# Kernel tuning notes

Measured on AMD Instinct MI355X. Metric: run time of the kernel, lower is better.

## Reference

```python
import jax, jax.numpy as jnp
import numpy as np

B, T, HID = 2, 2048, 2048
NH, NKV, HD = 32, 8, 64


def setup_inputs() -> dict:
    key = jax.random.key(0)
    ks = jax.random.split(key, 5)
    x = jax.random.normal(ks[0], (B, T, HID), dtype=jnp.float32)
    position_ids = jnp.broadcast_to(jnp.arange(T, dtype=jnp.int32), (B, T))
    s = 0.02
    Wq = jax.random.normal(ks[1], (NH * HD, HID), dtype=jnp.float32) * s
    Wk = jax.random.normal(ks[2], (NKV * HD, HID), dtype=jnp.float32) * s
    Wv = jax.random.normal(ks[3], (NKV * HD, HID), dtype=jnp.float32) * s
    Wo = jax.random.normal(ks[4], (HID, NH * HD), dtype=jnp.float32) * s
    return {"x": x, "position_ids": position_ids, "Wq": Wq, "Wk": Wk, "Wv": Wv, "Wo": Wo}


def _rotate_half(t):
    t1, t2 = jnp.split(t, 2, axis=-1)
    return jnp.concatenate([-t2, t1], axis=-1)


def reference(x, position_ids, Wq, Wk, Wv, Wo):
    Bd, Td, _ = x.shape
    q = (x @ Wq.T).reshape(Bd, Td, NH, HD)
    k = (x @ Wk.T).reshape(Bd, Td, NKV, HD)
    v = (x @ Wv.T).reshape(Bd, Td, NKV, HD)

    # DummyRotaryEmbedding: freqs over even indices, repeat_interleave(2)
    freqs = 1.0 / (10000.0 ** (jnp.arange(0, HD, 2, dtype=jnp.float32) / HD))
    angles = position_ids.astype(jnp.float32)[:, :, None] * freqs  # [B,T,HD/2]
    cos = jnp.repeat(jnp.cos(angles), 2, axis=-1)[:, :, None, :]   # [B,T,1,HD]
    sin = jnp.repeat(jnp.sin(angles), 2, axis=-1)[:, :, None, :]

    q = q * cos + _rotate_half(q) * sin
    k = k * cos + _rotate_half(k) * sin

    n_rep = NH // NKV
    k = jnp.repeat(k, n_rep, axis=2)  # [B,T,NH,HD]
    v = jnp.repeat(v, n_rep, axis=2)

    scale = 1.0 / np.sqrt(HD).astype(np.float32)
    scores = jnp.einsum('bqhd,bkhd->bhqk', q, k) * scale  # [B,NH,T,T]
    probs = jax.nn.softmax(scores, axis=-1)
    out = jnp.einsum('bhqk,bkhd->bqhd', probs, v).reshape(Bd, Td, NH * HD)
    return out @ Wo.T
```

## Files before the change

kernel.cpp:

```cpp
#include <hip/hip_runtime.h>
#include <hip/hip_bf16.h>
#include <stdint.h>


typedef __attribute__((ext_vector_type(8))) short short8;
typedef __attribute__((ext_vector_type(4))) float f32x4;
typedef __attribute__((ext_vector_type(16))) float f32x16;

__device__ __forceinline__ unsigned short f2bf(float f) {
  union { float f; uint32_t u; } x; x.f = f;
  uint32_t r = x.u + 0x7fffu + ((x.u >> 16) & 1u);
  return (unsigned short)(r >> 16);
}
__device__ __forceinline__ float bf2f(unsigned short u) {
  union { uint32_t u; float f; } x; x.u = ((uint32_t)u) << 16;
  return x.f;
}
__device__ __forceinline__ uint32_t cvt_pk_bf16(float a, float b) {
  uint32_t r;
  asm("v_cvt_pk_bf16_f32 %0, %1, %2" : "=v"(r) : "v"(a), "v"(b));
  return r;
}
__device__ __forceinline__ void pl32swap(uint32_t& dst, uint32_t& src) {
  asm("v_permlane32_swap_b32 %0, %1" : "+v"(dst), "+v"(src));
}

__device__ __forceinline__ void gload_lds16(const void* g, void* l) {
  __builtin_amdgcn_global_load_lds(
      (const __attribute__((address_space(1))) unsigned int*)g,
      (__attribute__((address_space(3))) unsigned int*)l, 16, 0, 0);
}

#define VMCNT(n) asm volatile("s_waitcnt vmcnt(" #n ")" ::: "memory")
#define LGKMCNT0 asm volatile("s_waitcnt lgkmcnt(0)" ::: "memory")

__global__ __launch_bounds__(256) void convert_kernel(
    const float* __restrict__ x, const float* __restrict__ Wq,
    const float* __restrict__ Wk, const float* __restrict__ Wv,
    const float* __restrict__ Wo,
    unsigned short* __restrict__ xb, unsigned short* __restrict__ wqkvb,
    unsigned short* __restrict__ wob) {
  const int NX = 1048576;
  const int NQ = 524288;
  const int NK = 131072;
  const int NV = 131072;
  const int NO = 524288;
  const int total = NX + NQ + NK + NV + NO;
  for (int i = blockIdx.x * blockDim.x + threadIdx.x; i < total;
       i += gridDim.x * blockDim.x) {
    const float4* s; unsigned short* d; int o;
    if (i < NX)                 { o = i;               s = (const float4*)x;  d = xb; }
    else if (i < NX+NQ)         { o = i-NX;            s = (const float4*)Wq; d = wqkvb; }
    else if (i < NX+NQ+NK)      { o = i-NX-NQ;         s = (const float4*)Wk; d = wqkvb + 4194304; }
    else if (i < NX+NQ+NK+NV)   { o = i-NX-NQ-NK;      s = (const float4*)Wv; d = wqkvb + 5242880; }
    else                        { o = i-NX-NQ-NK-NV;   s = (const float4*)Wo; d = wob; }
    float4 v0 = s[(size_t)o * 2];
    float4 v1 = s[(size_t)o * 2 + 1];
    short8 r;
    r[0] = (short)f2bf(v0.x); r[1] = (short)f2bf(v0.y);
    r[2] = (short)f2bf(v0.z); r[3] = (short)f2bf(v0.w);
    r[4] = (short)f2bf(v1.x); r[5] = (short)f2bf(v1.y);
    r[6] = (short)f2bf(v1.z); r[7] = (short)f2bf(v1.w);
    *(short8*)(d + (size_t)o * 8) = r;
  }
}

template <int NQ, typename OutT>
__global__ __launch_bounds__(512, 2) void gemm_2cu(
    const unsigned short* __restrict__ A, const unsigned short* __restrict__ Bt,
    OutT* __restrict__ C, int N, int K) {
  __shared__ unsigned short lA[2][128 * 64];
  __shared__ unsigned short lB[2][NQ * 64 * 64];
  const int tid  = threadIdx.x;
  const int lane = tid & 63;
  const int w    = tid >> 6;
  const int wr   = w >> 2, wc = w & 3;
  const long tm  = (long)blockIdx.y * 128;
  const long tn  = (long)blockIdx.x * (NQ * 64);

  f32x4 acc[4][NQ];
#pragma unroll
  for (int fi = 0; fi < 4; ++fi)
#pragma unroll
    for (int nq = 0; nq < NQ; ++nq) acc[fi][nq] = (f32x4){0.f, 0.f, 0.f, 0.f};

  const int srow = tid >> 3;
  const int sgr  = ((tid & 7) ^ (srow & 7)) * 8;
  const unsigned short* ga = A  + (tm + srow) * (long)K + sgr;
  const unsigned short* gb = Bt + (tn + srow) * (long)K + sgr;

  int aoff[4][2], boff[NQ][2];
#pragma unroll
  for (int fi = 0; fi < 4; ++fi)
#pragma unroll
    for (int ks = 0; ks < 2; ++ks) {
      int gk = (lane >> 4) + ks * 4;
      aoff[fi][ks] = (wr * 64 + fi * 16 + (lane & 15)) * 128 + ((gk ^ (lane & 7)) << 4);
    }
#pragma unroll
  for (int nq = 0; nq < NQ; ++nq)
#pragma unroll
    for (int ks = 0; ks < 2; ++ks) {
      int gk = (lane >> 4) + ks * 4;
      boff[nq][ks] = (wc * (NQ * 16) + nq * 16 + (lane & 15)) * 128 + ((gk ^ (lane & 7)) << 4);
    }

#pragma unroll
  for (int i = 0; i < 2; ++i)  gload_lds16(ga + (long)(64 * i) * K, &lA[0][tid * 8 + 4096 * i]);
#pragma unroll
  for (int i = 0; i < NQ; ++i) gload_lds16(gb + (long)(64 * i) * K, &lB[0][tid * 8 + 4096 * i]);
  VMCNT(0);
  __builtin_amdgcn_s_barrier();

  const int nk = K >> 6;
  for (int t = 0; t < nk; ++t) {
    const int slot = t & 1;
    const unsigned short* gaT = ga + (long)((t + 1) << 6);
    const unsigned short* gbT = gb + (long)((t + 1) << 6);
    const bool st = (t + 1 < nk);
    const char* As = (const char*)lA[slot];
    const char* Bs = (const char*)lB[slot];
    unsigned short* dA = &lA[slot ^ 1][tid * 8];
    unsigned short* dB = &lB[slot ^ 1][tid * 8];

    short8 af[4][2];
#pragma unroll
    for (int nq = 0; nq < NQ; ++nq) {
      if (nq == 0) {
#pragma unroll
        for (int fi = 0; fi < 4; ++fi)
#pragma unroll
          for (int ks = 0; ks < 2; ++ks)
            af[fi][ks] = *(const short8*)(As + aoff[fi][ks]);
      }
      short8 bf0 = *(const short8*)(Bs + boff[nq][0]);
      short8 bf1 = *(const short8*)(Bs + boff[nq][1]);
      if (st && nq == 0) {
        gload_lds16(gaT,                 dA);
        gload_lds16(gaT + (long)64 * K,  dA + 4096);
#pragma unroll
        for (int i = 0; i < NQ; ++i)
          gload_lds16(gbT + (long)(64 * i) * K, dB + 4096 * i);
      }
      __builtin_amdgcn_s_barrier();
      LGKMCNT0;
      __builtin_amdgcn_sched_barrier(0);
      __builtin_amdgcn_s_setprio(1);
#pragma unroll
      for (int fi = 0; fi < 4; ++fi)
        acc[fi][nq] = __builtin_amdgcn_mfma_f32_16x16x32_bf16(af[fi][0], bf0, acc[fi][nq], 0, 0, 0);
#pragma unroll
      for (int fi = 0; fi < 4; ++fi)
        acc[fi][nq] = __builtin_amdgcn_mfma_f32_16x16x32_bf16(af[fi][1], bf1, acc[fi][nq], 0, 0, 0);
      __builtin_amdgcn_s_setprio(0);
      __builtin_amdgcn_sched_barrier(0);
      if (nq == NQ - 1) VMCNT(0);
      __builtin_amdgcn_s_barrier();
    }
  }

#pragma unroll
  for (int fi = 0; fi < 4; ++fi)
#pragma unroll
    for (int nq = 0; nq < NQ; ++nq) {
      long col = tn + wc * (NQ * 16) + nq * 16 + (lane & 15);
#pragma unroll
      for (int i = 0; i < 4; ++i) {
        long row = tm + wr * 64 + fi * 16 + (lane >> 4) * 4 + i;
        float v = acc[fi][nq][i];
        if constexpr (sizeof(OutT) == 2) C[row * N + col] = (OutT)f2bf(v);
        else                             C[row * N + col] = (OutT)v;
      }
    }
}

__global__ __launch_bounds__(256) void rope_kernel(
    unsigned short* __restrict__ qkv, const int* __restrict__ pos_ids) {
  const int m = blockIdx.x;
  const int tid = threadIdx.x;
  const float QSCALE = 0.18033688011112042f;
  __shared__ float cs[32], sn[32];
  if (tid < 32) {
    float pos = (float)pos_ids[m];
    float a = pos * exp2f(-(float)tid * 0.4152410118609203f);
    float s_, c_;
    sincosf(a, &s_, &c_);
    cs[tid] = c_; sn[tid] = s_;
  }
  __syncthreads();
  unsigned short* row = qkv + (size_t)m * 3072;

  const int qc = tid * 8;
  short8 qa = *(const short8*)(row + qc);
  short8 qp = *(const short8*)(row + (qc ^ 32));
  short8 ka = {}, kp = {};
  if (tid < 64) {
    const int kc = 2048 + tid * 8;
    ka = *(const short8*)(row + kc);
    kp = *(const short8*)(row + (kc ^ 32));
  }
  __syncthreads();

  {
    const int dbase = qc & 63;
    const float sgn = (qc & 32) ? 1.0f : -1.0f;
    short8 out;
#pragma unroll
    for (int j = 0; j < 8; ++j) {
      int fi = (dbase + j) >> 1;
      float o = bf2f((unsigned short)qa[j]) * cs[fi] +
                sgn * bf2f((unsigned short)qp[j]) * sn[fi];
      out[j] = (short)f2bf(o * QSCALE);
    }
    *(short8*)(row + qc) = out;
  }
  if (tid < 64) {
    const int kc = 2048 + tid * 8;
    const int dbase = (tid * 8) & 63;
    const float sgn = ((tid * 8) & 32) ? 1.0f : -1.0f;
    short8 out;
#pragma unroll
    for (int j = 0; j < 8; ++j) {
      int fi = (dbase + j) >> 1;
      float o = bf2f((unsigned short)ka[j]) * cs[fi] +
                sgn * bf2f((unsigned short)kp[j]) * sn[fi];
      out[j] = (short)f2bf(o);
    }
    *(short8*)(row + kc) = out;
  }
}

__global__ __launch_bounds__(256) void vtrans_kernel(
    const unsigned short* __restrict__ qkv, unsigned short* __restrict__ Vt) {
  const int tb = blockIdx.x, g = blockIdx.y, b = blockIdx.z;
  const int tid = threadIdx.x;
  __shared__ unsigned short lt[64 * 72];

  {
    const int r = tid >> 2, c = (tid & 3) * 16;
    const unsigned short* src =
        qkv + ((size_t)(b * 2048 + tb * 64 + r)) * 3072 + 2560 + g * 64 + c;
    short8 v0 = *(const short8*)(src);
    short8 v1 = *(const short8*)(src + 8);
    *(short8*)&lt[r * 72 + c] = v0;
    *(short8*)&lt[r * 72 + c + 8] = v1;
  }
  __syncthreads();

  {
    const int d = tid >> 2, t0 = (tid & 3) * 16;
    short8 o0, o1;
#pragma unroll
    for (int j = 0; j < 8; ++j) o0[j] = (short)lt[(t0 + j) * 72 + d];
#pragma unroll
    for (int j = 0; j < 8; ++j) o1[j] = (short)lt[(t0 + 8 + j) * 72 + d];
    unsigned short* dst =
        Vt + ((size_t)((b * 8 + g) * 64 + d)) * 2048 + tb * 64 + t0;
    *(short8*)(dst) = o0;
    *(short8*)(dst + 8) = o1;
  }
}

__global__ __launch_bounds__(512) void attn_kernel(
    const unsigned short* __restrict__ qkv,
    const unsigned short* __restrict__ Vt,
    unsigned short* __restrict__ attnout) {
  const int qt = blockIdx.x, g = blockIdx.y, b = blockIdx.z;
  const int tid = threadIdx.x, lane = tid & 63, w = tid >> 6;
  const int l31 = lane & 31, hi = lane >> 5;
  const int h = g * 4 + (w & 3);
  const int qbase = qt * 64 + (w >> 2) * 32;

  __shared__ unsigned short lK[3][64 * 64];
  __shared__ unsigned short lV[4][64 * 64];

  short8 qf[4];
  {
    const unsigned short* qrow =
        qkv + ((size_t)(b * 2048 + qbase + l31)) * 3072 + h * 64 + hi * 8;
#pragma unroll
    for (int kc = 0; kc < 4; ++kc) qf[kc] = *(const short8*)(qrow + kc * 16);
  }

  f32x16 o0, o1, zro;
#pragma unroll
  for (int i = 0; i < 16; ++i) { o0[i] = 0.f; o1[i] = 0.f; zro[i] = 0.f; }
  float lrun = 0.f;

  const unsigned short* kgbase = qkv + (size_t)b * 2048 * 3072 + 2048 + g * 64;
  const unsigned short* vgbase = Vt + ((size_t)(b * 8 + g) * 64) * 2048;
  const int srow = w * 8 + (lane >> 3);
  const int sg = ((lane & 7) ^ (srow & 7)) * 8;

  int koff[2][4];
#pragma unroll
  for (int s = 0; s < 2; ++s)
#pragma unroll
    for (int kc = 0; kc < 4; ++kc) {
      int r = s * 32 + l31;
      koff[s][kc] = r * 128 + (((kc * 2 + hi) ^ (r & 7)) << 4);
    }

#define STAGE(kbuf, vbuf, kb)                                                       \
  {                                                                                 \
    const unsigned short* kk_ = kgbase + (size_t)((kb) * 64) * 3072;                \
    const unsigned short* vv_ = vgbase + (kb) * 64;                                 \
    gload_lds16(kk_ + (size_t)srow * 3072 + sg, &lK[kbuf][(w * 8) * 64]);           \
    gload_lds16(vv_ + (size_t)srow * 2048 + sg, &lV[vbuf][(w * 8) * 64]);           \
  }

#define PV_BLOCK(VBASE)                                                             \
  {                                                                                 \
    const char* Vb_ = (VBASE);                                                      \
    _Pragma("unroll")                                                               \
    for (int ks = 0; ks < 2; ++ks) {                                                \
      union { uint32_t u[4]; short8 s8; } fa, fb;                                   \
      _Pragma("unroll")                                                             \
      for (int u = 0; u < 4; ++u) { fa.u[u] = wd[ks][u]; fb.u[u] = wd[ks][4 + u]; } \
      const int kk0 = ks * 2, kk1 = ks * 2 + 1;                                     \
      short8 va0 = *(const short8*)(Vb_ + koff[0][kk0]);                            \
      short8 va1 = *(const short8*)(Vb_ + koff[1][kk0]);                            \
      o0 = __builtin_amdgcn_mfma_f32_32x32x16_bf16(fa.s8, va0, o0, 0, 0, 0);        \
      o1 = __builtin_amdgcn_mfma_f32_32x32x16_bf16(fa.s8, va1, o1, 0, 0, 0);        \
      short8 vb0 = *(const short8*)(Vb_ + koff[0][kk1]);                            \
      short8 vb1 = *(const short8*)(Vb_ + koff[1][kk1]);                            \
      o0 = __builtin_amdgcn_mfma_f32_32x32x16_bf16(fb.s8, vb0, o0, 0, 0, 0);        \
      o1 = __builtin_amdgcn_mfma_f32_32x32x16_bf16(fb.s8, vb1, o1, 0, 0, 0);        \
    }                                                                               \
  }

  uint32_t wd[2][8];

  STAGE(0, 0, 0);
  STAGE(1, 1, 1);
  VMCNT(2);
  __builtin_amdgcn_s_barrier();
  __builtin_amdgcn_sched_barrier(0);

  int kcur = 0;
  int kst  = 2;
#pragma unroll 1
  for (int t = 0; t < 32; ++t) {
    if (t < 30) STAGE(kst, (t + 2) & 3, t + 2);
    const char* Kb = (const char*)lK[kcur];

    f32x16 s0, s1;
    __builtin_amdgcn_s_setprio(1);
    {
      short8 k0 = *(const short8*)(Kb + koff[0][0]);
      short8 k1 = *(const short8*)(Kb + koff[1][0]);
      s0 = __builtin_amdgcn_mfma_f32_32x32x16_bf16(k0, qf[0], zro, 0, 0, 0);
      s1 = __builtin_amdgcn_mfma_f32_32x32x16_bf16(k1, qf[0], zro, 0, 0, 0);
    }
#pragma unroll
    for (int kc = 1; kc < 4; ++kc) {
      short8 k0 = *(const short8*)(Kb + koff[0][kc]);
      short8 k1 = *(const short8*)(Kb + koff[1][kc]);
      s0 = __builtin_amdgcn_mfma_f32_32x32x16_bf16(k0, qf[kc], s0, 0, 0, 0);
      s1 = __builtin_amdgcn_mfma_f32_32x32x16_bf16(k1, qf[kc], s1, 0, 0, 0);
    }
    if (t > 0) PV_BLOCK((const char*)lV[(t - 1) & 3]);
    __builtin_amdgcn_s_setprio(0);

#pragma unroll
    for (int i = 0; i < 16; ++i) { s0[i] = __builtin_amdgcn_exp2f(s0[i]); lrun += s0[i]; }
#pragma unroll
    for (int i = 0; i < 16; ++i) { s1[i] = __builtin_amdgcn_exp2f(s1[i]); lrun += s1[i]; }

#pragma unroll
    for (int mi = 0; mi < 8; ++mi) {
      wd[0][mi] = cvt_pk_bf16(s0[2 * mi], s0[2 * mi + 1]);
      wd[1][mi] = cvt_pk_bf16(s1[2 * mi], s1[2 * mi + 1]);
    }
#pragma unroll
    for (int ks = 0; ks < 2; ++ks) {
      pl32swap(wd[ks][0], wd[ks][2]);
      pl32swap(wd[ks][1], wd[ks][3]);
      pl32swap(wd[ks][4], wd[ks][6]);
      pl32swap(wd[ks][5], wd[ks][7]);
    }

    if (t < 30) { VMCNT(2); } else { VMCNT(0); }
    __builtin_amdgcn_s_barrier();
    __builtin_amdgcn_sched_barrier(0);

    kcur = (kcur == 2) ? 0 : kcur + 1;
    kst  = (kst == 2) ? 0 : kst + 1;
  }

  PV_BLOCK((const char*)lV[3]);

  lrun += __shfl_xor(lrun, 32);
  float inv = 1.0f / lrun;
  const size_t obase =
      (size_t)(b * 2048 + qbase) * 2048 + h * 64 + l31;
#pragma unroll
  for (int reg = 0; reg < 16; ++reg) {
    int q = (reg & 3) + 8 * (reg >> 2) + 4 * hi;
    float invq = __shfl(inv, q);
    attnout[obase + (size_t)q * 2048]      = f2bf(o0[reg] * invq);
    attnout[obase + (size_t)q * 2048 + 32] = f2bf(o1[reg] * invq);
  }
#undef STAGE
#undef PV_BLOCK
}

extern "C" void kernel_launch(void* const* d_in, const int* in_sizes, int n_in,
                              void* d_out, int out_size, void* d_ws, size_t ws_size,
                              hipStream_t stream) {
  (void)in_sizes; (void)n_in; (void)out_size; (void)ws_size;
  const float* x  = (const float*)d_in[0];
  const int* pos  = (const int*)d_in[1];
  const float* Wq = (const float*)d_in[2];
  const float* Wk = (const float*)d_in[3];
  const float* Wv = (const float*)d_in[4];
  const float* Wo = (const float*)d_in[5];
  float* out = (float*)d_out;
  char* ws = (char*)d_ws;

  unsigned short* xb      = (unsigned short*)(ws);
  unsigned short* wqkvb   = (unsigned short*)(ws + 16777216);
  unsigned short* wob     = (unsigned short*)(ws + 29360128);
  unsigned short* qkv     = (unsigned short*)(ws + 37748736);
  unsigned short* Vt      = (unsigned short*)(ws + 62914560);
  unsigned short* attnout = (unsigned short*)(ws + 67108864);

  convert_kernel<<<2048, 256, 0, stream>>>(x, Wq, Wk, Wv, Wo, xb, wqkvb, wob);
  gemm_2cu<3, unsigned short><<<dim3(16, 32), 512, 0, stream>>>(xb, wqkvb, qkv, 3072, 2048);
  rope_kernel<<<4096, 256, 0, stream>>>(qkv, pos);
  vtrans_kernel<<<dim3(32, 8, 2), 256, 0, stream>>>(qkv, Vt);
  attn_kernel<<<dim3(32, 8, 2), 512, 0, stream>>>(qkv, Vt, attnout);
  gemm_2cu<2, float><<<dim3(16, 32), 512, 0, stream>>>(attnout, wob, out, 2048, 2048);
}
```

Measured before the change: 195.9 us.

## Fuse fp32-to-bf16 weight conversion into GEMM B-operand loading

The weight conversion pass in the convert kernel is removed. Both GEMMs now read fp32 weights directly into registers, convert them to bf16 with packed cvt, and write them to LDS, double-buffered against the MFMA loop. This drops a separate read and write of about 10 MB of weights and shrinks the convert launch. In exchange, each GEMM block reads twice as many B bytes and repeats the conversion, because the weights are re-read by every M-tile block (32 row tiles). The B path also moves from async global_load_lds to register loads plus VALU work that must finish before the barrier.

Result: slower. 224.8 us (+14.8%).

```diff
diff --git a/kernel.cpp b/kernel.cpp
--- a/kernel.cpp
+++ b/kernel.cpp
@@ -35,39 +35,26 @@
 #define LGKMCNT0 asm volatile("s_waitcnt lgkmcnt(0)" ::: "memory")
 
 __global__ __launch_bounds__(256) void convert_kernel(
-    const float* __restrict__ x, const float* __restrict__ Wq,
-    const float* __restrict__ Wk, const float* __restrict__ Wv,
-    const float* __restrict__ Wo,
-    unsigned short* __restrict__ xb, unsigned short* __restrict__ wqkvb,
-    unsigned short* __restrict__ wob) {
+    const float* __restrict__ x, unsigned short* __restrict__ xb) {
   const int NX = 1048576;
-  const int NQ = 524288;
-  const int NK = 131072;
-  const int NV = 131072;
-  const int NO = 524288;
-  const int total = NX + NQ + NK + NV + NO;
-  for (int i = blockIdx.x * blockDim.x + threadIdx.x; i < total;
+  for (int i = blockIdx.x * blockDim.x + threadIdx.x; i < NX;
        i += gridDim.x * blockDim.x) {
-    const float4* s; unsigned short* d; int o;
-    if (i < NX)                 { o = i;               s = (const float4*)x;  d = xb; }
-    else if (i < NX+NQ)         { o = i-NX;            s = (const float4*)Wq; d = wqkvb; }
-    else if (i < NX+NQ+NK)      { o = i-NX-NQ;         s = (const float4*)Wk; d = wqkvb + 4194304; }
-    else if (i < NX+NQ+NK+NV)   { o = i-NX-NQ-NK;      s = (const float4*)Wv; d = wqkvb + 5242880; }
-    else                        { o = i-NX-NQ-NK-NV;   s = (const float4*)Wo; d = wob; }
-    float4 v0 = s[(size_t)o * 2];
-    float4 v1 = s[(size_t)o * 2 + 1];
+    const float4* s = (const float4*)x;
+    float4 v0 = s[(size_t)i * 2];
+    float4 v1 = s[(size_t)i * 2 + 1];
     short8 r;
     r[0] = (short)f2bf(v0.x); r[1] = (short)f2bf(v0.y);
     r[2] = (short)f2bf(v0.z); r[3] = (short)f2bf(v0.w);
     r[4] = (short)f2bf(v1.x); r[5] = (short)f2bf(v1.y);
     r[6] = (short)f2bf(v1.z); r[7] = (short)f2bf(v1.w);
-    *(short8*)(d + (size_t)o * 8) = r;
+    *(short8*)(xb + (size_t)i * 8) = r;
   }
 }
 
 template <int NQ, typename OutT>
-__global__ __launch_bounds__(512, 2) void gemm_2cu(
-    const unsigned short* __restrict__ A, const unsigned short* __restrict__ Bt,
+__global__ __launch_bounds__(512, 2) void gemm_cvtb(
+    const unsigned short* __restrict__ A, const float* __restrict__ B0,
+    const float* __restrict__ B1, const float* __restrict__ B2,
     OutT* __restrict__ C, int N, int K) {
   __shared__ unsigned short lA[2][128 * 64];
   __shared__ unsigned short lB[2][NQ * 64 * 64];
@@ -86,8 +73,18 @@
 
   const int srow = tid >> 3;
   const int sgr  = ((tid & 7) ^ (srow & 7)) * 8;
-  const unsigned short* ga = A  + (tm + srow) * (long)K + sgr;
-  const unsigned short* gb = Bt + (tn + srow) * (long)K + sgr;
+  const unsigned short* ga = A + (tm + srow) * (long)K + sgr;
+
+  const float* bsrc[NQ];
+#pragma unroll
+  for (int i = 0; i < NQ; ++i) {
+    long rn = tn + srow + 64 * i;
+    const float* base;
+    if (B1 != nullptr && rn >= 2560)      base = B2 + (size_t)(rn - 2560) * K;
+    else if (B1 != nullptr && rn >= 2048) base = B1 + (size_t)(rn - 2048) * K;
+    else                                  base = B0 + (size_t)rn * K;
+    bsrc[i] = base + sgr;
+  }
 
   int aoff[4][2], boff[NQ][2];
 #pragma unroll
@@ -105,23 +102,41 @@
       boff[nq][ks] = (wc * (NQ * 16) + nq * 16 + (lane & 15)) * 128 + ((gk ^ (lane & 7)) << 4);
     }
 
+  float4 bl[NQ][2];
+
+#define BCVT(slot_)                                                          \
+  {                                                                          \
+    _Pragma("unroll")                                                        \
+    for (int i = 0; i < NQ; ++i) {                                           \
+      union { uint32_t u[4]; short8 s8; } cw;                                \
+      cw.u[0] = cvt_pk_bf16(bl[i][0].x, bl[i][0].y);                         \
+      cw.u[1] = cvt_pk_bf16(bl[i][0].z, bl[i][0].w);                         \
+      cw.u[2] = cvt_pk_bf16(bl[i][1].x, bl[i][1].y);                         \
+      cw.u[3] = cvt_pk_bf16(bl[i][1].z, bl[i][1].w);                         \
+      *(short8*)&lB[slot_][tid * 8 + 4096 * i] = cw.s8;                      \
+    }                                                                        \
+  }
+
 #pragma unroll
   for (int i = 0; i < 2; ++i)  gload_lds16(ga + (long)(64 * i) * K, &lA[0][tid * 8 + 4096 * i]);
 #pragma unroll
-  for (int i = 0; i < NQ; ++i) gload_lds16(gb + (long)(64 * i) * K, &lB[0][tid * 8 + 4096 * i]);
+  for (int i = 0; i < NQ; ++i) {
+    bl[i][0] = *(const float4*)(bsrc[i]);
+    bl[i][1] = *(const float4*)(bsrc[i] + 4);
+  }
   VMCNT(0);
+  BCVT(0);
+  LGKMCNT0;
   __builtin_amdgcn_s_barrier();
 
   const int nk = K >> 6;
   for (int t = 0; t < nk; ++t) {
     const int slot = t & 1;
-    const unsigned short* gaT = ga + (long)((t + 1) << 6);
-    const unsigned short* gbT = gb + (long)((t + 1) << 6);
+    const long ktn = (long)((t + 1) << 6);
     const bool st = (t + 1 < nk);
     const char* As = (const char*)lA[slot];
     const char* Bs = (const char*)lB[slot];
     unsigned short* dA = &lA[slot ^ 1][tid * 8];
-    unsigned short* dB = &lB[slot ^ 1][tid * 8];
 
     short8 af[4][2];
 #pragma unroll
@@ -136,11 +151,13 @@
       short8 bf0 = *(const short8*)(Bs + boff[nq][0]);
       short8 bf1 = *(const short8*)(Bs + boff[nq][1]);
       if (st && nq == 0) {
-        gload_lds16(gaT,                 dA);
-        gload_lds16(gaT + (long)64 * K,  dA + 4096);
-#pragma unroll
-        for (int i = 0; i < NQ; ++i)
-          gload_lds16(gbT + (long)(64 * i) * K, dB + 4096 * i);
+        gload_lds16(ga + ktn,                 dA);
+        gload_lds16(ga + ktn + (long)64 * K,  dA + 4096);
+#pragma unroll
+        for (int i = 0; i < NQ; ++i) {
+          bl[i][0] = *(const float4*)(bsrc[i] + ktn);
+          bl[i][1] = *(const float4*)(bsrc[i] + ktn + 4);
+        }
       }
       __builtin_amdgcn_s_barrier();
       LGKMCNT0;
@@ -154,7 +171,11 @@
         acc[fi][nq] = __builtin_amdgcn_mfma_f32_16x16x32_bf16(af[fi][1], bf1, acc[fi][nq], 0, 0, 0);
       __builtin_amdgcn_s_setprio(0);
       __builtin_amdgcn_sched_barrier(0);
-      if (nq == NQ - 1) VMCNT(0);
+      if (nq == NQ - 1 && st) {
+        VMCNT(0);
+        BCVT(slot ^ 1);
+        LGKMCNT0;
+      }
       __builtin_amdgcn_s_barrier();
     }
   }
@@ -172,6 +193,7 @@
         else                             C[row * N + col] = (OutT)v;
       }
     }
+#undef BCVT
 }
 
 __global__ __launch_bounds__(256) void rope_kernel(
@@ -419,16 +441,16 @@
   char* ws = (char*)d_ws;
 
   unsigned short* xb      = (unsigned short*)(ws);
-  unsigned short* wqkvb   = (unsigned short*)(ws + 16777216);
-  unsigned short* wob     = (unsigned short*)(ws + 29360128);
   unsigned short* qkv     = (unsigned short*)(ws + 37748736);
   unsigned short* Vt      = (unsigned short*)(ws + 62914560);
   unsigned short* attnout = (unsigned short*)(ws + 67108864);
 
-  convert_kernel<<<2048, 256, 0, stream>>>(x, Wq, Wk, Wv, Wo, xb, wqkvb, wob);
-  gemm_2cu<3, unsigned short><<<dim3(16, 32), 512, 0, stream>>>(xb, wqkvb, qkv, 3072, 2048);
+  convert_kernel<<<1024, 256, 0, stream>>>(x, xb);
+  gemm_cvtb<3, unsigned short><<<dim3(16, 32), 512, 0, stream>>>(
+      xb, Wq, Wk, Wv, qkv, 3072, 2048);
   rope_kernel<<<4096, 256, 0, stream>>>(qkv, pos);
   vtrans_kernel<<<dim3(32, 8, 2), 256, 0, stream>>>(qkv, Vt);
   attn_kernel<<<dim3(32, 8, 2), 512, 0, stream>>>(qkv, Vt, attnout);
-  gemm_2cu<2, float><<<dim3(16, 32), 512, 0, stream>>>(attnout, wob, out, 2048, 2048);
-}
+  gemm_cvtb<2, float><<<dim3(16, 32), 512, 0, stream>>>(
+      attnout, Wo, nullptr, nullptr, out, 2048, 2048);
+}
```
